# Kernel tuning notes

Measured on AMD Instinct MI355X. Metric: run time of the kernel, lower is better.

The kernel has to match this reference:

```python
import jax, jax.numpy as jnp
import numpy as np

HEATMAP_SIZE = 64

def _gauss5():
    n = np.array([[1, 4, 7, 4, 1],
                  [4, 16, 26, 16, 4],
                  [7, 26, 41, 26, 7],
                  [4, 16, 26, 16, 4],
                  [1, 4, 7, 4, 1]], dtype=np.float32) / 41.0
    return n

def setup_inputs() -> dict:
    key = jax.random.key(0)
    k1, k2, k3 = jax.random.split(key, 3)
    B, K = 1024, 24
    # coords in [-1.2, 1.2] so a few land out of the heatmap and exercise the masking path
    x = jax.random.uniform(k1, (B, K, 2), jnp.float32, -1.2, 1.2)
    # every (out,in) filter slice is the same 5x5 binomial gaussian (as in weights_init)
    weight = jnp.asarray(np.broadcast_to(_gauss5(), (K, K, 5, 5)).copy())
    vis_batch = jax.random.randint(k2, (256,), 0, B, jnp.int32)
    vis_kps = jax.random.randint(k3, (256,), 0, K, jnp.int32)
    return {"x": x, "weight": weight, "vis_batch": vis_batch, "vis_kps": vis_kps}

def _forward(x, weight, vis_batch, vis_kps):
    B, K, _ = x.shape
    H = HEATMAP_SIZE
    # j2d_resized = round((j2d + 1) / 2 * (H - 1)).long()
    coords = jnp.round((x + 1.0) * 0.5 * (H - 1)).astype(jnp.int32)  # [B,K,2] = (x,y)
    # rows with any out-of-range coord get both coords set to 0
    invalid = jnp.any((coords >= H) | (coords < 0), axis=-1)  # [B,K]
    coords = jnp.where(invalid[..., None], 0, coords)
    # torch quirk: only places a 1 where the x-coordinate is nonzero
    place = (coords[..., 0] != 0).astype(weight.dtype)  # [B,K]
    ohx = jax.nn.one_hot(coords[..., 0], H, dtype=weight.dtype)  # [B,K,H]
    ohy = jax.nn.one_hot(coords[..., 1], H, dtype=weight.dtype)  # [B,K,H]
    # sparse heatmap: 1 at (y, x)
    heat = place[..., None, None] * ohy[..., :, None] * ohx[..., None, :]  # [B,K,H,H]
    # heatmap[vis_batch, vis_kps, :, :] = 0
    kill = jnp.zeros((B, K), weight.dtype).at[vis_batch, vis_kps].set(1.0)
    heat = heat * (1.0 - kill)[..., None, None]
    # full 24->24 channel-mixing 5x5 conv, padding=2, no bias
    out = jax.lax.conv_general_dilated(
        heat, weight, window_strides=(1, 1), padding=((2, 2), (2, 2)),
        dimension_numbers=("NCHW", "OIHW", "NCHW"))
    return out

def reference(x, weight, vis_batch, vis_kps):
    return _forward(x, weight, vis_batch, vis_kps)
```

## Files before the change

### kernel.cpp

```cpp
#include <hip/hip_runtime.h>
#include <math.h>

#define B_SZ 1024
#define K_SZ 24
#define H_SZ 64
#define NVIS 256

__global__ __launch_bounds__(256) void gs_main(
    const float* __restrict__ x,
    const float* __restrict__ w,
    const int*   __restrict__ vis_b,
    const int*   __restrict__ vis_k,
    float*       __restrict__ out)
{
    __shared__ float tile[H_SZ * H_SZ];
    __shared__ int   spike[K_SZ];

    const int bid = blockIdx.x;
    const int b   = bid / K_SZ;
    const int o   = bid - b * K_SZ;
    const int tid = threadIdx.x;

#pragma unroll
    for (int i = 0; i < 16; ++i) tile[i * 256 + tid] = 0.0f;

    if (tid < K_SZ) {
        float fx = x[(b * K_SZ + tid) * 2 + 0];
        float fy = x[(b * K_SZ + tid) * 2 + 1];
        int cx = (int)rintf((fx + 1.0f) * 0.5f * 63.0f);
        int cy = (int)rintf((fy + 1.0f) * 0.5f * 63.0f);
        bool in_range = (cx >= 0) & (cx < H_SZ) & (cy >= 0) & (cy < H_SZ);
        bool placed = in_range && (cx != 0);
        spike[tid] = placed ? (cy * H_SZ + cx) : -1;
    }
    __syncthreads();

    {
        int vb = vis_b[tid];
        if (vb == b) spike[vis_k[tid]] = -1;
    }
    __syncthreads();

    for (int t = tid; t < K_SZ * 25; t += 256) {
        int c = t / 25;
        int p = t - c * 25;
        int s = spike[c];
        if (s >= 0) {
            int y  = s >> 6;
            int xx = s & 63;
            int di = p / 5;
            int dj = p - di * 5;
            int i = y + 2 - di;
            int j = xx + 2 - dj;
            if (((unsigned)i < H_SZ) & ((unsigned)j < H_SZ)) {
                float wv = w[((o * K_SZ + c) * 5 + di) * 5 + dj];
                atomicAdd(&tile[i * H_SZ + j], wv);
            }
        }
    }
    __syncthreads();

    float4*       o4 = (float4*)(out + (size_t)bid * (H_SZ * H_SZ));
    const float4* t4 = (const float4*)tile;
#pragma unroll
    for (int r = 0; r < 4; ++r) o4[r * 256 + tid] = t4[r * 256 + tid];
}

extern "C" void kernel_launch(void* const* d_in, const int* in_sizes, int n_in,
                              void* d_out, int out_size, void* d_ws, size_t ws_size,
                              hipStream_t stream) {
    const float* x     = (const float*)d_in[0];
    const float* w     = (const float*)d_in[1];
    const int*   vis_b = (const int*)d_in[2];
    const int*   vis_k = (const int*)d_in[3];
    float*       out   = (float*)d_out;

    gs_main<<<B_SZ * K_SZ, 256, 0, stream>>>(x, w, vis_b, vis_k, out);
}
```

Before: 417.0 us.

## Precompute spike table in a prep kernel and prefetch weights before tile clear

Adds a small prep kernel that computes each (batch, keypoint) spike position once, including the visibility kill, and writes it to workspace. The previously redundant per-output-channel coordinate math and two barriers are removed. The main kernel now issues its spike and weight loads into registers before zeroing the tile with float4 stores, so global load latency overlaps the clear. It costs an extra kernel launch plus a workspace round trip. The main kernel is bound by output writes, so the gain may be small.

```diff
diff --git a/kernel.cpp b/kernel.cpp
--- a/kernel.cpp
+++ b/kernel.cpp
@@ -6,74 +6,91 @@
 #define H_SZ 64
 #define NVIS 256
 
+
+__global__ __launch_bounds__(256) void gs_prep(
+    const float2* __restrict__ x,
+    const int*    __restrict__ vis_b,
+    const int*    __restrict__ vis_k,
+    int*          __restrict__ spike_tab)
+{
+    const int bk = blockIdx.x * 256 + threadIdx.x;
+    const int b  = bk / K_SZ;
+    const int k  = bk - b * K_SZ;
+    const float2 c = x[bk];
+    const int cx = (int)rintf((c.x + 1.0f) * 0.5f * 63.0f);
+    const int cy = (int)rintf((c.y + 1.0f) * 0.5f * 63.0f);
+    const bool ok = (cx >= 1) & (cx < H_SZ) & (cy >= 0) & (cy < H_SZ);
+    int s = ok ? (cy * H_SZ + cx) : -1;
+    for (int i = 0; i < NVIS; ++i) {
+        if ((vis_b[i] == b) & (vis_k[i] == k)) s = -1;
+    }
+    spike_tab[bk] = s;
+}
+
 __global__ __launch_bounds__(256) void gs_main(
-    const float* __restrict__ x,
+    const int*   __restrict__ spike_tab,
     const float* __restrict__ w,
-    const int*   __restrict__ vis_b,
-    const int*   __restrict__ vis_k,
     float*       __restrict__ out)
 {
     __shared__ float tile[H_SZ * H_SZ];
-    __shared__ int   spike[K_SZ];
-
     const int bid = blockIdx.x;
     const int b   = bid / K_SZ;
     const int o   = bid - b * K_SZ;
     const int tid = threadIdx.x;
 
-#pragma unroll
-    for (int i = 0; i < 16; ++i) tile[i * 256 + tid] = 0.0f;
+    const int*   sp = spike_tab + b * K_SZ;
+    const float* wo = w + o * (K_SZ * 25);
+    int   sv[3]; float wv[3]; int pp[3];
+    #pragma unroll
+    for (int it = 0; it < 3; ++it) {
+        const int t = tid + it * 256;
+        if (t < K_SZ * 25) {
+            const int c = t / 25;
+            pp[it] = t - c * 25;
+            sv[it] = sp[c];
+            wv[it] = wo[t];
+        } else {
+            sv[it] = -1;
+        }
+    }
 
-    if (tid < K_SZ) {
-        float fx = x[(b * K_SZ + tid) * 2 + 0];
-        float fy = x[(b * K_SZ + tid) * 2 + 1];
-        int cx = (int)rintf((fx + 1.0f) * 0.5f * 63.0f);
-        int cy = (int)rintf((fy + 1.0f) * 0.5f * 63.0f);
-        bool in_range = (cx >= 0) & (cx < H_SZ) & (cy >= 0) & (cy < H_SZ);
-        bool placed = in_range && (cx != 0);
-        spike[tid] = placed ? (cy * H_SZ + cx) : -1;
-    }
+    float4* t4 = (float4*)tile;
+    const float4 z = make_float4(0.f, 0.f, 0.f, 0.f);
+    #pragma unroll
+    for (int r = 0; r < 4; ++r) t4[r * 256 + tid] = z;
     __syncthreads();
 
-    {
-        int vb = vis_b[tid];
-        if (vb == b) spike[vis_k[tid]] = -1;
-    }
-    __syncthreads();
-
-    for (int t = tid; t < K_SZ * 25; t += 256) {
-        int c = t / 25;
-        int p = t - c * 25;
-        int s = spike[c];
+    #pragma unroll
+    for (int it = 0; it < 3; ++it) {
+        const int s = sv[it];
         if (s >= 0) {
-            int y  = s >> 6;
-            int xx = s & 63;
-            int di = p / 5;
-            int dj = p - di * 5;
-            int i = y + 2 - di;
-            int j = xx + 2 - dj;
-            if (((unsigned)i < H_SZ) & ((unsigned)j < H_SZ)) {
-                float wv = w[((o * K_SZ + c) * 5 + di) * 5 + dj];
-                atomicAdd(&tile[i * H_SZ + j], wv);
-            }
+            const int y  = s >> 6;
+            const int xx = s & 63;
+            const int di = pp[it] / 5;
+            const int dj = pp[it] - di * 5;
+            const int i  = y + 2 - di;
+            const int j  = xx + 2 - dj;
+            if (((unsigned)i < H_SZ) & ((unsigned)j < H_SZ))
+                atomicAdd(&tile[i * H_SZ + j], wv[it]);
         }
     }
     __syncthreads();
 
-    float4*       o4 = (float4*)(out + (size_t)bid * (H_SZ * H_SZ));
-    const float4* t4 = (const float4*)tile;
-#pragma unroll
+    float4* o4 = (float4*)(out + (size_t)bid * (H_SZ * H_SZ));
+    #pragma unroll
     for (int r = 0; r < 4; ++r) o4[r * 256 + tid] = t4[r * 256 + tid];
 }
 
 extern "C" void kernel_launch(void* const* d_in, const int* in_sizes, int n_in,
                               void* d_out, int out_size, void* d_ws, size_t ws_size,
                               hipStream_t stream) {
-    const float* x     = (const float*)d_in[0];
-    const float* w     = (const float*)d_in[1];
-    const int*   vis_b = (const int*)d_in[2];
-    const int*   vis_k = (const int*)d_in[3];
-    float*       out   = (float*)d_out;
+    const float2* x     = (const float2*)d_in[0];
+    const float*  w     = (const float*)d_in[1];
+    const int*    vis_b = (const int*)d_in[2];
+    const int*    vis_k = (const int*)d_in[3];
+    float*        out   = (float*)d_out;
+    int*          spike_tab = (int*)d_ws;
 
-    gs_main<<<B_SZ * K_SZ, 256, 0, stream>>>(x, w, vis_b, vis_k, out);
+    gs_prep<<<(B_SZ * K_SZ) / 256, 256, 0, stream>>>(x, vis_b, vis_k, spike_tab);
+    gs_main<<<B_SZ * K_SZ, 256, 0, stream>>>(spike_tab, w, out);
 }
```

Result: faster. 401.4 us (-3.7%).
